# Performance work log

Hardware: AMD Instinct MI355X
Metric: run time of the kernel (lower is better)

## Reference

```python
import jax, jax.numpy as jnp
import numpy as np

NODES = 16384                       # power of two -> all heap levels complete
DEPTH = (NODES - 1).bit_length() + 1  # 15 heap steps, linears k = 0..14
IN_F = 64
OUT_F = 64
MINHEAP = 0
BATCH = 32


def setup_inputs() -> dict:
    key = jax.random.key(0)
    k1, k2, k3 = jax.random.split(key, 3)
    x = jax.random.normal(k1, (BATCH, NODES, IN_F), dtype=jnp.float32)
    # stacked per-heap-step Linear params, torch layout W: [out, in]
    W = jax.random.normal(k2, (DEPTH - MINHEAP, OUT_F, IN_F), dtype=jnp.float32) * 0.05
    b = jax.random.normal(k3, (DEPTH - MINHEAP, OUT_F), dtype=jnp.float32) * 0.05
    return {"x": x, "W": W, "b": b}


def reference(x, W, b):
    # HeapLinear forward. Heap layout: level l occupies nodes [2^(l-1), 2^l)
    # (root = node 0, level(j) = bit_length(j)). The original double loop over
    # (input level l, linear k) with repeat_interleave(2^k) is equivalent to:
    #   output[j] = sum_{k=minheap}^{depth-1, level(j)>=k} linears[k](input[j >> k])
    # for power-of-two `nodes` (every out block satisfies out_node1 <= nodes).
    nodes = x.shape[-2]
    depth = (nodes - 1).bit_length() + 1
    j = np.arange(nodes)
    levels = np.array([int(v).bit_length() for v in j])  # static, trace-time
    out = jnp.zeros(x.shape[:-1] + (W.shape[1],), dtype=x.dtype)
    for k in range(MINHEAP, depth):
        n_anc = max(nodes >> k, 1)  # only nodes 0..n_anc-1 serve as distance-k ancestors
        # small per-level Linear applied to ancestor slice: [..., n_anc, out]
        t = jnp.einsum('...ni,oi->...no', x[..., :n_anc, :], W[k - MINHEAP]) + b[k - MINHEAP]
        anc = j >> k                      # distance-k ancestor of each node
        mask = levels >= k                # nodes shallower than k have no such ancestor
        out = out + jnp.where(mask[:, None], t[..., anc, :], jnp.zeros((), x.dtype))
    return out
```

## Files before the change

kernel.cpp:

```cpp
#include <hip/hip_runtime.h>

#define NODES 16384
#define NF 64
#define NBLK 128
#define SROW 72
#define SROWS 270
#define TROW 72
#define BATCH 32

typedef __attribute__((ext_vector_type(8))) short short8;
typedef __attribute__((ext_vector_type(4))) short shortx4;
typedef __attribute__((ext_vector_type(4))) float floatx4;

__device__ __forceinline__ short f2bf(float f) {
    unsigned u = __float_as_uint(f);
    u += 0x7fffu + ((u >> 16) & 1u);
    return (short)(u >> 16);
}
__device__ __forceinline__ float bf2f(short s) {
    return __uint_as_float(((unsigned)(unsigned short)s) << 16);
}
__device__ __forceinline__ short8 loadW8(const float* p) {
    floatx4 a = *(const floatx4*)(p);
    floatx4 b = *(const floatx4*)(p + 4);
    short8 r;
    r[0]=f2bf(a[0]); r[1]=f2bf(a[1]); r[2]=f2bf(a[2]); r[3]=f2bf(a[3]);
    r[4]=f2bf(b[0]); r[5]=f2bf(b[1]); r[6]=f2bf(b[2]); r[7]=f2bf(b[3]);
    return r;
}

__global__ __launch_bounds__(256, 4)
void heaplin_kernel(const float* __restrict__ x, const float* __restrict__ W,
                    const float* __restrict__ bias, float* __restrict__ out)
{
    __shared__ short stage[SROWS * SROW];
    __shared__ float farpart[4 * 64];
    short* tbuf = stage;
    float* cumB = (float*)(stage + 128 * SROW);

    const int tid  = threadIdx.x;
    const int lane = tid & 63;
    const int wave = tid >> 6;
    const int lr = lane & 15;
    const int lq = lane >> 4;
    const int nblk = blockIdx.x;
    const int b    = blockIdx.y;
    const float* xb = x + (size_t)b * NODES * NF;
    float* ob = out + (size_t)b * NODES * NF;
    const floatx4 zero4 = {0.f, 0.f, 0.f, 0.f};

    if (nblk == 0) {
        if (tid < 64) {
            float run = 0.f;
            for (int k = 0; k < 15; ++k) { run += bias[k * 64 + tid]; cumB[k * 64 + tid] = run; }
        }
        floatx4 accE[8];
        #pragma unroll
        for (int t8 = 0; t8 < 8; ++t8) accE[t8] = zero4;

        for (int k = 0; k < 8; ++k) {
            __syncthreads();
            #pragma unroll
            for (int i = 0; i < 8; ++i) {
                int job = tid + i * 256;
                int r = job >> 4, c4 = job & 15;
                bool valid = (k == 0) || (r >= (1 << (k - 1)));
                floatx4 vv = zero4;
                if (valid) vv = *(const floatx4*)(xb + (r >> k) * NF + c4 * 4);
                shortx4 s4;
                s4[0]=f2bf(vv[0]); s4[1]=f2bf(vv[1]); s4[2]=f2bf(vv[2]); s4[3]=f2bf(vv[3]);
                *(shortx4*)(stage + r * SROW + c4 * 4) = s4;
            }
            __syncthreads();
            #pragma unroll
            for (int t8 = 0; t8 < 8; ++t8) {
                int mt = 2 * wave + (t8 & 1);
                int nt = t8 >> 1;
                int arow = mt * 16 + lr;
                const float* wr = W + k * 4096 + (nt * 16 + lr) * 64 + lq * 8;
                short8 b0 = loadW8(wr);
                short8 b1 = loadW8(wr + 32);
                short8 a0 = *(const short8*)(stage + arow * SROW + lq * 8);
                short8 a1 = *(const short8*)(stage + arow * SROW + 32 + lq * 8);
                accE[t8] = __builtin_amdgcn_mfma_f32_16x16x32_bf16(a0, b0, accE[t8], 0, 0, 0);
                accE[t8] = __builtin_amdgcn_mfma_f32_16x16x32_bf16(a1, b1, accE[t8], 0, 0, 0);
            }
        }
        #pragma unroll
        for (int t8 = 0; t8 < 8; ++t8) {
            int mt = 2 * wave + (t8 & 1);
            int nt = t8 >> 1;
            int c = nt * 16 + lr;
            #pragma unroll
            for (int rg = 0; rg < 4; ++rg) {
                int j = mt * 16 + lq * 4 + rg;
                int lvl = (j == 0) ? 0 : (32 - __clz(j));
                ob[(size_t)j * NF + c] = accE[t8][rg] + cumB[lvl * 64 + c];
            }
        }
        return;
    }

    const int n0 = nblk * NBLK;
    const int L  = 32 - __clz(n0);

    floatx4 v[16];
    #pragma unroll
    for (int i = 0; i < 16; ++i) {
        int job = tid + i * 256;
        int r = job >> 4, c4 = job & 15;
        int node;
        if (r < 128)        node = n0 + r;
        else if (r >= 254)  node = n0 >> 7;
        else { int k = __clz(255 - r) - 24; node = (n0 >> k) + r - (256 - (256 >> k)); }
        v[i] = *(const floatx4*)(xb + (size_t)node * NF + c4 * 4);
    }
    #pragma unroll
    for (int i = 0; i < 16; ++i) {
        int job = tid + i * 256;
        int r = job >> 4, c4 = job & 15;
        shortx4 s4;
        s4[0]=f2bf(v[i][0]); s4[1]=f2bf(v[i][1]); s4[2]=f2bf(v[i][2]); s4[3]=f2bf(v[i][3]);
        *(shortx4*)(stage + r * SROW + c4 * 4) = s4;
    }
    __syncthreads();

    floatx4 accE[8];
    #pragma unroll
    for (int t8 = 0; t8 < 8; ++t8) {
        int mt = 2 * wave + (t8 & 1);
        int nt = t8 >> 1;
        int arow = mt * 16 + lr;
        const float* wr = W + (nt * 16 + lr) * 64 + lq * 8;
        short8 b0 = loadW8(wr);
        short8 b1 = loadW8(wr + 32);
        short8 a0 = *(const short8*)(stage + arow * SROW + lq * 8);
        short8 a1 = *(const short8*)(stage + arow * SROW + 32 + lq * 8);
        floatx4 acc = zero4;
        acc = __builtin_amdgcn_mfma_f32_16x16x32_bf16(a0, b0, acc, 0, 0, 0);
        acc = __builtin_amdgcn_mfma_f32_16x16x32_bf16(a1, b1, acc, 0, 0, 0);
        accE[t8] = acc;
    }

    {
        float p = 0.f;
        const int q = wave, o = lane;
        for (int k = 8; k <= L; ++k) {
            const float* xa = xb + (size_t)(n0 >> k) * NF + q * 16;
            const float* wr = W + k * 4096 + o * 64 + q * 16;
            #pragma unroll
            for (int i = 0; i < 4; ++i) {
                floatx4 wv = *(const floatx4*)(wr + i * 4);
                floatx4 xv = *(const floatx4*)(xa + i * 4);
                p += wv[0]*xv[0] + wv[1]*xv[1] + wv[2]*xv[2] + wv[3]*xv[3];
            }
        }
        if (q == 0) for (int k = 0; k <= L; ++k) p += bias[k * 64 + o];
        farpart[q * 64 + o] = p;
    }
    __syncthreads();

    for (int jj = 0; jj < 11; ++jj) {
        int job = wave + jj * 4;
        int idx = job % 11;
        int nt  = job / 11;
        int k, mt;
        if (idx < 4)      { k = 1; mt = idx; }
        else if (idx < 6) { k = 2; mt = idx - 4; }
        else if (idx < 7) { k = 3; mt = 0; }
        else              { k = idx - 3; mt = 0; }
        int sbase = 256 - (256 >> k);
        int arow = sbase + mt * 16 + lr;
        const float* wr = W + k * 4096 + (nt * 16 + lr) * 64 + lq * 8;
        short8 b0 = loadW8(wr);
        short8 b1 = loadW8(wr + 32);
        short8 a0 = *(const short8*)(stage + arow * SROW + lq * 8);
        short8 a1 = *(const short8*)(stage + arow * SROW + 32 + lq * 8);
        floatx4 acc = zero4;
        acc = __builtin_amdgcn_mfma_f32_16x16x32_bf16(a0, b0, acc, 0, 0, 0);
        acc = __builtin_amdgcn_mfma_f32_16x16x32_bf16(a1, b1, acc, 0, 0, 0);
        int tb = 128 - (256 >> k);
        int nvalid = 128 >> k;
        #pragma unroll
        for (int rg = 0; rg < 4; ++rg) {
            int m = mt * 16 + lq * 4 + rg;
            if (m < nvalid) tbuf[(tb + m) * TROW + nt * 16 + lr] = f2bf(acc[rg]);
        }
    }
    __syncthreads();

    {
        int m  = tid >> 2;
        int c0 = (tid & 3) * 16;
        float e[16];
        #pragma unroll
        for (int i = 0; i < 16; ++i) {
            int c = c0 + i;
            e[i] = bf2f(tbuf[ m              * TROW + c])
                 + bf2f(tbuf[(64  + (m >> 1)) * TROW + c])
                 + bf2f(tbuf[(96  + (m >> 2)) * TROW + c])
                 + bf2f(tbuf[(112 + (m >> 3)) * TROW + c])
                 + bf2f(tbuf[(120 + (m >> 4)) * TROW + c])
                 + bf2f(tbuf[(124 + (m >> 5)) * TROW + c])
                 + bf2f(tbuf[126              * TROW + c])
                 + farpart[c] + farpart[64 + c] + farpart[128 + c] + farpart[192 + c];
        }
        #pragma unroll
        for (int i = 0; i < 16; ++i) tbuf[m * TROW + c0 + i] = f2bf(e[i]);
    }
    __syncthreads();

    #pragma unroll
    for (int t8 = 0; t8 < 8; ++t8) {
        int mt = 2 * wave + (t8 & 1);
        int nt = t8 >> 1;
        int c = nt * 16 + lr;
        #pragma unroll
        for (int rg = 0; rg < 4; ++rg) {
            int j = mt * 16 + lq * 4 + rg;
            float val = accE[t8][rg] + bf2f(tbuf[(j >> 1) * TROW + c]);
            ob[(size_t)(n0 + j) * NF + c] = val;
        }
    }
}

extern "C" void kernel_launch(void* const* d_in, const int* in_sizes, int n_in,
                              void* d_out, int out_size, void* d_ws, size_t ws_size,
                              hipStream_t stream) {
    const float* x  = (const float*)d_in[0];
    const float* W  = (const float*)d_in[1];
    const float* bs = (const float*)d_in[2];
    float* out = (float*)d_out;
    dim3 grid(NODES / NBLK, BATCH);
    heaplin_kernel<<<grid, 256, 0, stream>>>(x, W, bs, out);
}
```

Measured before the change: 392.7 us.

## Add bf16 pre-swizzle pass for x and W, MFMA operands loaded directly

```diff
diff --git a/kernel.cpp b/kernel.cpp
--- a/kernel.cpp
+++ b/kernel.cpp
@@ -3,10 +3,13 @@
 #define NODES 16384
 #define NF 64
 #define NBLK 128
-#define SROW 72
-#define SROWS 270
 #define TROW 72
 #define BATCH 32
+
+#define WS_XSWZ_OFF   0ull
+#define WS_WBF_OFF    67108864ull
+#define WS_BPRE_OFF   67231744ull
+#define WS_NEEDED     67235584ull
 
 typedef __attribute__((ext_vector_type(8))) short short8;
 typedef __attribute__((ext_vector_type(4))) short shortx4;
@@ -20,18 +23,223 @@
 __device__ __forceinline__ float bf2f(short s) {
     return __uint_as_float(((unsigned)(unsigned short)s) << 16);
 }
-__device__ __forceinline__ short8 loadW8(const float* p) {
-    floatx4 a = *(const floatx4*)(p);
-    floatx4 b = *(const floatx4*)(p + 4);
+__device__ __forceinline__ short8 cvt8(floatx4 a, floatx4 c) {
     short8 r;
     r[0]=f2bf(a[0]); r[1]=f2bf(a[1]); r[2]=f2bf(a[2]); r[3]=f2bf(a[3]);
-    r[4]=f2bf(b[0]); r[5]=f2bf(b[1]); r[6]=f2bf(b[2]); r[7]=f2bf(b[3]);
+    r[4]=f2bf(c[0]); r[5]=f2bf(c[1]); r[6]=f2bf(c[2]); r[7]=f2bf(c[3]);
     return r;
 }
 
+__global__ __launch_bounds__(256)
+void heaplin_prep(const float* __restrict__ x, const float* __restrict__ W,
+                  const float* __restrict__ bias,
+                  short* __restrict__ xswz, short* __restrict__ wbf,
+                  float* __restrict__ bpre)
+{
+    const int blk = blockIdx.x;
+    const int tid = threadIdx.x;
+    if (blk < 16384) {
+        int g  = blk * 256 + tid;
+        int p  = g & 127;
+        int tg = g >> 7;
+        const float* src = x + ((size_t)(tg << 4) + (p & 15)) * NF + (p >> 4) * 8;
+        floatx4 a = *(const floatx4*)src;
+        floatx4 c = *(const floatx4*)(src + 4);
+        *(short8*)(xswz + (size_t)g * 8) = cvt8(a, c);
+    } else if (blk < 16414) {
+        int e = (blk - 16384) * 2048 + tid * 8;
+        floatx4 a = *(const floatx4*)(W + e);
+        floatx4 c = *(const floatx4*)(W + e + 4);
+        *(short8*)(wbf + e) = cvt8(a, c);
+    } else {
+        if (tid < 64) {
+            float run = 0.f;
+            for (int k = 0; k < 15; ++k) { run += bias[k * 64 + tid]; bpre[k * 64 + tid] = run; }
+        }
+    }
+}
+
 __global__ __launch_bounds__(256, 4)
-void heaplin_kernel(const float* __restrict__ x, const float* __restrict__ W,
-                    const float* __restrict__ bias, float* __restrict__ out)
+void heaplin_main(const float* __restrict__ x, const float* __restrict__ W,
+                  const short* __restrict__ xswz, const short* __restrict__ wbf,
+                  const float* __restrict__ bpre, float* __restrict__ out)
+{
+    __shared__ short tbuf[128 * TROW];
+    __shared__ float farpart[4 * 64];
+
+    const int tid  = threadIdx.x;
+    const int lane = tid & 63;
+    const int wave = tid >> 6;
+    const int lr = lane & 15;
+    const int lq = lane >> 4;
+    const int nblk = blockIdx.x;
+    const int b    = blockIdx.y;
+    const float* xb = x + (size_t)b * NODES * NF;
+    const short* xsb = xswz + (size_t)b * NODES * NF;
+    float* ob = out + (size_t)b * NODES * NF;
+    const floatx4 zero4 = {0.f, 0.f, 0.f, 0.f};
+
+    if (nblk == 0) {
+        floatx4 accE[8];
+        #pragma unroll
+        for (int t8 = 0; t8 < 8; ++t8) accE[t8] = zero4;
+
+        for (int k = 0; k < 8; ++k) {
+            __syncthreads();
+            #pragma unroll
+            for (int i = 0; i < 8; ++i) {
+                int job = tid + i * 256;
+                int r = job >> 4, c4 = job & 15;
+                bool valid = (k == 0) || (r >= (1 << (k - 1)));
+                floatx4 vv = zero4;
+                if (valid) vv = *(const floatx4*)(xb + (r >> k) * NF + c4 * 4);
+                shortx4 s4;
+                s4[0]=f2bf(vv[0]); s4[1]=f2bf(vv[1]); s4[2]=f2bf(vv[2]); s4[3]=f2bf(vv[3]);
+                *(shortx4*)(tbuf + r * TROW + c4 * 4) = s4;
+            }
+            __syncthreads();
+            #pragma unroll
+            for (int t8 = 0; t8 < 8; ++t8) {
+                int mt = 2 * wave + (t8 & 1);
+                int nt = t8 >> 1;
+                int arow = mt * 16 + lr;
+                const short* wp = wbf + k * 4096 + (nt * 16 + lr) * 64 + lq * 8;
+                short8 b0 = *(const short8*)wp;
+                short8 b1 = *(const short8*)(wp + 32);
+                short8 a0 = *(const short8*)(tbuf + arow * TROW + lq * 8);
+                short8 a1 = *(const short8*)(tbuf + arow * TROW + 32 + lq * 8);
+                accE[t8] = __builtin_amdgcn_mfma_f32_16x16x32_bf16(a0, b0, accE[t8], 0, 0, 0);
+                accE[t8] = __builtin_amdgcn_mfma_f32_16x16x32_bf16(a1, b1, accE[t8], 0, 0, 0);
+            }
+        }
+        #pragma unroll
+        for (int t8 = 0; t8 < 8; ++t8) {
+            int mt = 2 * wave + (t8 & 1);
+            int nt = t8 >> 1;
+            int c = nt * 16 + lr;
+            #pragma unroll
+            for (int rg = 0; rg < 4; ++rg) {
+                int j = mt * 16 + lq * 4 + rg;
+                int lvl = (j == 0) ? 0 : (32 - __clz(j));
+                ob[(size_t)j * NF + c] = accE[t8][rg] + bpre[lvl * 64 + c];
+            }
+        }
+        return;
+    }
+
+    const int n0 = nblk * NBLK;
+    const int L  = 32 - __clz(n0);
+
+    floatx4 accE[8];
+    const short* xtile0 = xsb + (size_t)(n0 >> 4) * 1024;
+    #pragma unroll
+    for (int t8 = 0; t8 < 8; ++t8) {
+        int mt = 2 * wave + (t8 & 1);
+        int nt = t8 >> 1;
+        const short* ap = xtile0 + mt * 1024 + lane * 8;
+        short8 a0 = *(const short8*)ap;
+        short8 a1 = *(const short8*)(ap + 512);
+        const short* wp = wbf + (nt * 16 + lr) * 64 + lq * 8;
+        short8 b0 = *(const short8*)wp;
+        short8 b1 = *(const short8*)(wp + 32);
+        floatx4 acc = zero4;
+        acc = __builtin_amdgcn_mfma_f32_16x16x32_bf16(a0, b0, acc, 0, 0, 0);
+        acc = __builtin_amdgcn_mfma_f32_16x16x32_bf16(a1, b1, acc, 0, 0, 0);
+        accE[t8] = acc;
+    }
+
+    {
+        float p = 0.f;
+        const int q = wave, o = lane;
+        for (int k = 8; k <= L; ++k) {
+            const float* xa = xb + (size_t)(n0 >> k) * NF + q * 16;
+            const float* wr = W + k * 4096 + o * 64 + q * 16;
+            #pragma unroll
+            for (int i = 0; i < 4; ++i) {
+                floatx4 wv = *(const floatx4*)(wr + i * 4);
+                floatx4 xv = *(const floatx4*)(xa + i * 4);
+                p += wv[0]*xv[0] + wv[1]*xv[1] + wv[2]*xv[2] + wv[3]*xv[3];
+            }
+        }
+        if (q == 0) p += bpre[L * 64 + o];
+        farpart[q * 64 + o] = p;
+    }
+
+    for (int jj = 0; jj < 11; ++jj) {
+        int job = wave * 11 + jj;
+        int idx = job >> 2;
+        int nt  = job & 3;
+        int k, mt;
+        if (idx < 4)       { k = 1; mt = idx; }
+        else if (idx < 6)  { k = 2; mt = idx - 4; }
+        else if (idx == 6) { k = 3; mt = 0; }
+        else               { k = idx - 3; mt = 0; }
+        int anc = n0 >> k;
+        int T   = (anc >> 4) + mt;
+        int off = anc & 15;
+        const short* ap = xsb + (size_t)T * 1024 + lane * 8;
+        short8 a0 = *(const short8*)ap;
+        short8 a1 = *(const short8*)(ap + 512);
+        const short* wp = wbf + k * 4096 + (nt * 16 + lr) * 64 + lq * 8;
+        short8 b0 = *(const short8*)wp;
+        short8 b1 = *(const short8*)(wp + 32);
+        floatx4 acc = zero4;
+        acc = __builtin_amdgcn_mfma_f32_16x16x32_bf16(a0, b0, acc, 0, 0, 0);
+        acc = __builtin_amdgcn_mfma_f32_16x16x32_bf16(a1, b1, acc, 0, 0, 0);
+        int tb  = 128 - (256 >> k);
+        int cnt = 128 >> k;
+        #pragma unroll
+        for (int rg = 0; rg < 4; ++rg) {
+            int m = lq * 4 + rg;
+            if (k <= 3) {
+                tbuf[(tb + mt * 16 + m) * TROW + nt * 16 + lr] = f2bf(acc[rg]);
+            } else if (m >= off && m < off + cnt) {
+                tbuf[(tb + m - off) * TROW + nt * 16 + lr] = f2bf(acc[rg]);
+            }
+        }
+    }
+    __syncthreads();
+
+    {
+        int m  = tid >> 2;
+        int c0 = (tid & 3) * 16;
+        float e[16];
+        #pragma unroll
+        for (int i = 0; i < 16; ++i) {
+            int c = c0 + i;
+            e[i] = bf2f(tbuf[ m               * TROW + c])
+                 + bf2f(tbuf[(64  + (m >> 1)) * TROW + c])
+                 + bf2f(tbuf[(96  + (m >> 2)) * TROW + c])
+                 + bf2f(tbuf[(112 + (m >> 3)) * TROW + c])
+                 + bf2f(tbuf[(120 + (m >> 4)) * TROW + c])
+                 + bf2f(tbuf[(124 + (m >> 5)) * TROW + c])
+                 + bf2f(tbuf[126              * TROW + c])
+                 + farpart[c] + farpart[64 + c] + farpart[128 + c] + farpart[192 + c];
+        }
+        #pragma unroll
+        for (int i = 0; i < 16; ++i) tbuf[m * TROW + c0 + i] = f2bf(e[i]);
+    }
+    __syncthreads();
+
+    #pragma unroll
+    for (int t8 = 0; t8 < 8; ++t8) {
+        int mt = 2 * wave + (t8 & 1);
+        int nt = t8 >> 1;
+        int c = nt * 16 + lr;
+        #pragma unroll
+        for (int rg = 0; rg < 4; ++rg) {
+            int j = mt * 16 + lq * 4 + rg;
+            float val = accE[t8][rg] + bf2f(tbuf[(j >> 1) * TROW + c]);
+            ob[(size_t)(n0 + j) * NF + c] = val;
+        }
+    }
+}
+
+#define SROW 72
+#define SROWS 270
+__global__ __launch_bounds__(256, 4)
+void heaplin_fallback(const float* __restrict__ x, const float* __restrict__ W,
+                      const float* __restrict__ bias, float* __restrict__ out)
 {
     __shared__ short stage[SROWS * SROW];
     __shared__ float farpart[4 * 64];
@@ -57,7 +265,6 @@
         floatx4 accE[8];
         #pragma unroll
         for (int t8 = 0; t8 < 8; ++t8) accE[t8] = zero4;
-
         for (int k = 0; k < 8; ++k) {
             __syncthreads();
             #pragma unroll
@@ -78,8 +285,10 @@
                 int nt = t8 >> 1;
                 int arow = mt * 16 + lr;
                 const float* wr = W + k * 4096 + (nt * 16 + lr) * 64 + lq * 8;
-                short8 b0 = loadW8(wr);
-                short8 b1 = loadW8(wr + 32);
+                floatx4 wa = *(const floatx4*)wr, wb2 = *(const floatx4*)(wr + 4);
+                short8 b0 = cvt8(wa, wb2);
+                floatx4 wc = *(const floatx4*)(wr + 32), wd = *(const floatx4*)(wr + 36);
+                short8 b1 = cvt8(wc, wd);
                 short8 a0 = *(const short8*)(stage + arow * SROW + lq * 8);
                 short8 a1 = *(const short8*)(stage + arow * SROW + 32 + lq * 8);
                 accE[t8] = __builtin_amdgcn_mfma_f32_16x16x32_bf16(a0, b0, accE[t8], 0, 0, 0);
@@ -103,7 +312,6 @@
 
     const int n0 = nblk * NBLK;
     const int L  = 32 - __clz(n0);
-
     floatx4 v[16];
     #pragma unroll
     for (int i = 0; i < 16; ++i) {
@@ -124,7 +332,6 @@
         *(shortx4*)(stage + r * SROW + c4 * 4) = s4;
     }
     __syncthreads();
-
     floatx4 accE[8];
     #pragma unroll
     for (int t8 = 0; t8 < 8; ++t8) {
@@ -132,8 +339,10 @@
         int nt = t8 >> 1;
         int arow = mt * 16 + lr;
         const float* wr = W + (nt * 16 + lr) * 64 + lq * 8;
-        short8 b0 = loadW8(wr);
-        short8 b1 = loadW8(wr + 32);
+        floatx4 wa = *(const floatx4*)wr, wb2 = *(const floatx4*)(wr + 4);
+        short8 b0 = cvt8(wa, wb2);
+        floatx4 wc = *(const floatx4*)(wr + 32), wd = *(const floatx4*)(wr + 36);
+        short8 b1 = cvt8(wc, wd);
         short8 a0 = *(const short8*)(stage + arow * SROW + lq * 8);
         short8 a1 = *(const short8*)(stage + arow * SROW + 32 + lq * 8);
         floatx4 acc = zero4;
@@ -141,7 +350,6 @@
         acc = __builtin_amdgcn_mfma_f32_16x16x32_bf16(a1, b1, acc, 0, 0, 0);
         accE[t8] = acc;
     }
-
     {
         float p = 0.f;
         const int q = wave, o = lane;
@@ -159,7 +367,6 @@
         farpart[q * 64 + o] = p;
     }
     __syncthreads();
-
     for (int jj = 0; jj < 11; ++jj) {
         int job = wave + jj * 4;
         int idx = job % 11;
@@ -172,8 +379,10 @@
         int sbase = 256 - (256 >> k);
         int arow = sbase + mt * 16 + lr;
         const float* wr = W + k * 4096 + (nt * 16 + lr) * 64 + lq * 8;
-        short8 b0 = loadW8(wr);
-        short8 b1 = loadW8(wr + 32);
+        floatx4 wa = *(const floatx4*)wr, wb2 = *(const floatx4*)(wr + 4);
+        short8 b0 = cvt8(wa, wb2);
+        floatx4 wc = *(const floatx4*)(wr + 32), wd = *(const floatx4*)(wr + 36);
+        short8 b1 = cvt8(wc, wd);
         short8 a0 = *(const short8*)(stage + arow * SROW + lq * 8);
         short8 a1 = *(const short8*)(stage + arow * SROW + 32 + lq * 8);
         floatx4 acc = zero4;
@@ -188,7 +397,6 @@
         }
     }
     __syncthreads();
-
     {
         int m  = tid >> 2;
         int c0 = (tid & 3) * 16;
@@ -196,7 +404,7 @@
         #pragma unroll
         for (int i = 0; i < 16; ++i) {
             int c = c0 + i;
-            e[i] = bf2f(tbuf[ m              * TROW + c])
+            e[i] = bf2f(tbuf[ m               * TROW + c])
                  + bf2f(tbuf[(64  + (m >> 1)) * TROW + c])
                  + bf2f(tbuf[(96  + (m >> 2)) * TROW + c])
                  + bf2f(tbuf[(112 + (m >> 3)) * TROW + c])
@@ -209,7 +417,6 @@
         for (int i = 0; i < 16; ++i) tbuf[m * TROW + c0 + i] = f2bf(e[i]);
     }
     __syncthreads();
-
     #pragma unroll
     for (int t8 = 0; t8 < 8; ++t8) {
         int mt = 2 * wave + (t8 & 1);
@@ -232,5 +439,13 @@
     const float* bs = (const float*)d_in[2];
     float* out = (float*)d_out;
     dim3 grid(NODES / NBLK, BATCH);
-    heaplin_kernel<<<grid, 256, 0, stream>>>(x, W, bs, out);
-}
+    if (ws_size >= WS_NEEDED) {
+        short* xswz = (short*)((char*)d_ws + WS_XSWZ_OFF);
+        short* wbf  = (short*)((char*)d_ws + WS_WBF_OFF);
+        float* bpre = (float*)((char*)d_ws + WS_BPRE_OFF);
+        heaplin_prep<<<16415, 256, 0, stream>>>(x, W, bs, xswz, wbf, bpre);
+        heaplin_main<<<grid, 256, 0, stream>>>(x, W, xswz, wbf, bpre, out);
+    } else {
+        heaplin_fallback<<<grid, 256, 0, stream>>>(x, W, bs, out);
+    }
+}
```

After: 359.7 us. 8.4% less time.
